# Performance work log

Hardware: AMD Instinct MI355X
Metric: run time of the kernel (lower is better)

## Reference

```python
import jax, jax.numpy as jnp
import numpy as np
from jax import lax

DIM = 128      # per-head dim == channel dim of input
HEADS = 8
INNER = DIM * HEADS
KSZ = 3        # proj_kernel
PAD = KSZ // 2
B = 8
X = 4096       # sequence length
EPS = 1e-5     # BatchNorm eps
SCALE = DIM ** -0.5


def _dw_block(x, dw_w, bn_g, bn_b, bn_m, bn_v, pw_w, pad):
    """DepthWiseConv1d: depthwise conv -> eval-mode BN -> 1x1 conv (no bias).
    x: (n, dim, L); dw_w: (dim, 1, k); pw_w: (out, dim)."""
    dim = dw_w.shape[0]
    y = lax.conv_general_dilated(x, dw_w, (1,), [(pad, pad)],
                                 dimension_numbers=('NCH', 'OIH', 'NCH'),
                                 feature_group_count=dim)
    y = (y - bn_m[:, None]) * (bn_g[:, None] * lax.rsqrt(bn_v[:, None] + EPS)) + bn_b[:, None]
    return jnp.einsum('oi,nix->nox', pw_w, y)


def setup_inputs() -> dict:
    key = jax.random.key(0)
    ks = iter(jax.random.split(key, 40))
    d = {'x': jax.random.normal(next(ks), (B, DIM, X), dtype=jnp.float32)}
    for p in ('q', 'k', 'v'):
        d[p + '_dw'] = jax.random.normal(next(ks), (DIM, 1, KSZ), dtype=jnp.float32) * 0.3
        d[p + '_g'] = 1.0 + 0.1 * jax.random.normal(next(ks), (DIM,), dtype=jnp.float32)
        d[p + '_b'] = 0.1 * jax.random.normal(next(ks), (DIM,), dtype=jnp.float32)
        d[p + '_m'] = 0.1 * jax.random.normal(next(ks), (DIM,), dtype=jnp.float32)
        d[p + '_v'] = jax.random.uniform(next(ks), (DIM,), dtype=jnp.float32, minval=0.5, maxval=1.5)
        d[p + '_pw'] = jax.random.normal(next(ks), (INNER, DIM), dtype=jnp.float32) * (DIM ** -0.5)
    # gating DWConv (dim -> dim, kernel 1, no bias)
    d['gt_dw'] = jax.random.normal(next(ks), (DIM, 1, 1), dtype=jnp.float32) * 0.3
    d['gt_g'] = 1.0 + 0.1 * jax.random.normal(next(ks), (DIM,), dtype=jnp.float32)
    d['gt_b'] = 0.1 * jax.random.normal(next(ks), (DIM,), dtype=jnp.float32)
    d['gt_m'] = 0.1 * jax.random.normal(next(ks), (DIM,), dtype=jnp.float32)
    d['gt_v'] = jax.random.uniform(next(ks), (DIM,), dtype=jnp.float32, minval=0.5, maxval=1.5)
    d['gt_pw'] = jax.random.normal(next(ks), (DIM, DIM), dtype=jnp.float32) * (DIM ** -0.5)
    # to_out 1x1 conv (inner -> dim) with bias
    d['out_w'] = jax.random.normal(next(ks), (DIM, INNER), dtype=jnp.float32) * (INNER ** -0.5)
    d['out_b'] = 0.1 * jax.random.normal(next(ks), (DIM,), dtype=jnp.float32)
    return d


def _split_heads(t):
    # (b, h*d, x) -> (b*h, x, d)
    return t.reshape(B, HEADS, DIM, X).transpose(0, 1, 3, 2).reshape(B * HEADS, X, DIM)


def reference(x, q_dw, q_g, q_b, q_m, q_v, q_pw,
              k_dw, k_g, k_b, k_m, k_v, k_pw,
              v_dw, v_g, v_b, v_m, v_v, v_pw,
              gt_dw, gt_g, gt_b, gt_m, gt_v, gt_pw,
              out_w, out_b):
    q = _split_heads(_dw_block(x, q_dw, q_g, q_b, q_m, q_v, q_pw, PAD))  # (n, x, d)
    k = _split_heads(_dw_block(x, k_dw, k_g, k_b, k_m, k_v, k_pw, PAD))
    v = _split_heads(_dw_block(x, v_dw, v_g, v_b, v_m, v_v, v_pw, PAD))
    # k <- q^T @ softmax(k, axis=-1) * scale : (n, d, d)
    kat = jnp.einsum('nxd,nxe->nde', q, jax.nn.softmax(k, axis=-1)) * SCALE
    # gate: sigmoid(DWConv(q^T)^T) * v
    g_out = _dw_block(q.transpose(0, 2, 1), gt_dw, gt_g, gt_b, gt_m, gt_v, gt_pw, 0)  # (n, d, x)
    gate = jax.nn.sigmoid(g_out.transpose(0, 2, 1)) * v                  # (n, x, d)
    out = jnp.einsum('nxd,nde->nxe', v, kat) + gate                      # (n, x, d)
    out = out.reshape(B, HEADS, X, DIM).transpose(0, 1, 3, 2).reshape(B, INNER, X)
    return jnp.einsum('oi,nix->nox', out_w, out) + out_b[:, None]        # (b, dim, x)
```

## Files before the change

### kernel.cpp

```cpp
#include <hip/hip_runtime.h>
#include <hip/hip_bf16.h>

#define DIMC   128
#define HEADS  8
#define BATCH  8
#define XLEN   4096
#define NHEAD  64
#define EPSV   1e-5f
#define SCALEF 0.08838834764831845f
#define TX     64

typedef __attribute__((ext_vector_type(8))) short bf16x8;
typedef __attribute__((ext_vector_type(4))) float f32x4;
#define MFMA(a,b,c) __builtin_amdgcn_mfma_f32_16x16x32_bf16((a),(b),(c),0,0,0)
#define LDW(tbl, kt, nt) (*(const bf16x8*)&(tbl)[(((kt) * 8 + (nt)) * 64 + l) * 8])

__device__ __forceinline__ short f2bf(float f) {
  union { float f; unsigned u; } v; v.f = f;
  return (short)((v.u + 0x7fffu + ((v.u >> 16) & 1u)) >> 16);
}
__device__ __forceinline__ float bf2f(short h) {
  union { unsigned u; float f; } v; v.u = ((unsigned)(unsigned short)h) << 16;
  return v.f;
}
__device__ __forceinline__ unsigned pk2(float a, float b) {
  return (unsigned)(unsigned short)f2bf(a) | ((unsigned)(unsigned short)f2bf(b) << 16);
}

__device__ __forceinline__ bf16x8 ldY(const short* Y, int row, int kcb) {
  return *(const bf16x8*)((const char*)Y + row*256 + (kcb ^ ((row&7)<<4)));
}

__global__ void k_prep1(const float* dw0, const float* g0, const float* b0, const float* m0, const float* v0,
                        const float* dw1, const float* g1, const float* b1, const float* m1, const float* v1,
                        const float* dw2, const float* g2, const float* b2, const float* m2, const float* v2,
                        const float* gt_pw, const float* gt_dw, const float* gt_g,
                        const float* gt_b, const float* gt_m, const float* gt_v,
                        float* __restrict__ dwf, float* __restrict__ bfl,
                        float* __restrict__ Gt, float* __restrict__ c0) {
  int p = blockIdx.x, c = threadIdx.x;
  if (p < 3) {
    const float* dw = p == 0 ? dw0 : p == 1 ? dw1 : dw2;
    const float* g  = p == 0 ? g0  : p == 1 ? g1  : g2;
    const float* bb = p == 0 ? b0  : p == 1 ? b1  : b2;
    const float* m  = p == 0 ? m0  : p == 1 ? m1  : m2;
    const float* vv = p == 0 ? v0  : p == 1 ? v1  : v2;
    float a = g[c] * rsqrtf(vv[c] + EPSV);
    dwf[(p * DIMC + c) * 3 + 0] = dw[c * 3 + 0] * a;
    dwf[(p * DIMC + c) * 3 + 1] = dw[c * 3 + 1] * a;
    dwf[(p * DIMC + c) * 3 + 2] = dw[c * 3 + 2] * a;
    bfl[p * DIMC + c] = bb[c] - m[c] * a;
  } else {
    int d = c;
    float s = 0.f;
    for (int i = 0; i < DIMC; ++i) {
      float a  = gt_g[i] * rsqrtf(gt_v[i] + EPSV);
      float w1 = gt_dw[i] * a;
      float w0 = gt_b[i] - gt_m[i] * a;
      float pw = gt_pw[d * DIMC + i];
      Gt[i * DIMC + d] = pw * w1;
      s += pw * w0;
    }
    c0[d] = s;
  }
}

__global__ void k_wg(const float* __restrict__ q_pw, const float* __restrict__ Gt,
                     float* __restrict__ WgF) {
  const int h = blockIdx.x, cb = blockIdx.y, t = threadIdx.x;
  const int c = cb * 16 + (t >> 4);
  const int e0 = (t & 15) * 8;
  float acc[8] = {0.f,0.f,0.f,0.f,0.f,0.f,0.f,0.f};
  for (int d = 0; d < DIMC; ++d) {
    float wq = q_pw[((size_t)(h * DIMC + d)) * DIMC + c];
    const float* gr = Gt + d * DIMC + e0;
    #pragma unroll
    for (int j = 0; j < 8; ++j) acc[j] += wq * gr[j];
  }
  float* out = WgF + ((size_t)h * DIMC + c) * DIMC + e0;
  #pragma unroll
  for (int j = 0; j < 8; ++j) out[j] = acc[j];
}

__global__ void k_pack(const float* __restrict__ q_pw, const float* __restrict__ k_pw,
                       const float* __restrict__ v_pw, const float* __restrict__ out_w,
                       const float* __restrict__ WgF,
                       short* __restrict__ Wpk, short* __restrict__ Opk,
                       short* __restrict__ Gpk) {
  const int blk = blockIdx.x, t = threadIdx.x;
  if (blk < 48) {
    const int p = blk / 16, h = (blk / 2) & 7, hl = blk & 1;
    const float* pw = p == 0 ? q_pw : p == 1 ? k_pw : v_pw;
    short* dst = Wpk + (size_t)((p * 8 + h) * 2 + hl) * 16384;
    for (int s = t; s < 2048; s += 256) {
      const int l = s & 63, kt = (s >> 6) >> 3, nt = (s >> 6) & 7;
      const int o = h * DIMC + nt * 16 + (l & 15);
      const int cb = kt * 32 + (l >> 4) * 8;
      #pragma unroll
      for (int j = 0; j < 8; ++j) {
        float wv = pw[(size_t)o * DIMC + cb + j];
        short hi = f2bf(wv);
        dst[s * 8 + j] = (hl == 0) ? hi : f2bf(wv - bf2f(hi));
      }
    }
  } else if (blk < 64) {
    const int m = blk - 48, h = m >> 1, hl = m & 1;
    short* dst = Opk + (size_t)(h * 2 + hl) * 16384;
    for (int s = t; s < 2048; s += 256) {
      const int l = s & 63, mt = (s >> 6) >> 2, kt = (s >> 6) & 3;
      const int o = mt * 16 + (l & 15);
      const int ib = h * DIMC + kt * 32 + (l >> 4) * 8;
      #pragma unroll
      for (int j = 0; j < 8; ++j) {
        float wv = out_w[(size_t)o * (DIMC * HEADS) + ib + j];
        short hi = f2bf(wv);
        dst[s * 8 + j] = (hl == 0) ? hi : f2bf(wv - bf2f(hi));
      }
    }
  } else {
    const int h = blk - 64;
    const float* src = WgF + (size_t)h * 16384;
    short* dst = Gpk + (size_t)h * 16384;
    for (int s = t; s < 2048; s += 256) {
      const int l = s & 63, kt = (s >> 6) >> 3, nt = (s >> 6) & 7;
      const int cb = kt * 32 + (l >> 4) * 8, e = nt * 16 + (l & 15);
      #pragma unroll
      for (int j = 0; j < 8; ++j) dst[s * 8 + j] = f2bf(src[(size_t)(cb + j) * DIMC + e]);
    }
  }
}

__global__ __launch_bounds__(256) void k_red(const short* __restrict__ part16,
                                             short* __restrict__ katpk, int splits) {
  __shared__ float sm[DIMC * DIMC];
  const int n = blockIdx.x, t = threadIdx.x;
  for (int i0 = t * 8; i0 < DIMC * DIMC; i0 += 256 * 8) {
    float a[8] = {0.f,0.f,0.f,0.f,0.f,0.f,0.f,0.f};
    for (int s8 = 0; s8 < splits; ++s8) {
      bf16x8 pv = *(const bf16x8*)&part16[((size_t)(s8 * NHEAD + n)) * 16384 + i0];
      #pragma unroll
      for (int j = 0; j < 8; ++j) a[j] += bf2f(pv[j]);
    }
    #pragma unroll
    for (int j = 0; j < 8; ++j) sm[i0 + j] = a[j] * SCALEF;
  }
  __syncthreads();
  short* dst = katpk + (size_t)n * 16384;
  for (int s = t; s < 2048; s += 256) {
    const int l = s & 63, kt = (s >> 6) >> 3, nt = (s >> 6) & 7;
    const int db = kt * 32 + (l >> 4) * 8, e = nt * 16 + (l & 15);
    #pragma unroll
    for (int j = 0; j < 8; ++j) dst[s * 8 + j] = f2bf(sm[(db + j) * DIMC + e]);
  }
}

__device__ __forceinline__ void stage2(const float* __restrict__ x,
    const float* __restrict__ dwf, const float* __restrict__ bfl,
    int b, int xg0, int t, short* Y0, short* Y1, int p0, int p1)
{
  const int xl = t & 63, cg = t >> 6;
  const int xg = xg0 + xl;
  #pragma unroll
  for (int i = 0; i < 16; ++i) {
    const int c = 2 * (cg + 4 * i);
    float v0[2], v1[2];
    #pragma unroll
    for (int u = 0; u < 2; ++u) {
      const int cc = c + u;
      const float* xr = x + ((size_t)b * DIMC + cc) * XLEN + xg;
      float xm = (xg > 0) ? xr[-1] : 0.f;
      float xc = xr[0];
      float xp = (xg < XLEN - 1) ? xr[1] : 0.f;
      const float* d0 = dwf + (p0 * DIMC + cc) * 3;
      const float* d1 = dwf + (p1 * DIMC + cc) * 3;
      v0[u] = xm * d0[0] + xc * d0[1] + xp * d0[2] + bfl[p0 * DIMC + cc];
      v1[u] = xm * d1[0] + xc * d1[1] + xp * d1[2] + bfl[p1 * DIMC + cc];
    }
    const unsigned off = xl * 256 + ((c * 2) ^ ((xl & 7) << 4));
    *(unsigned*)((char*)Y0 + off) = pk2(v0[0], v0[1]);
    *(unsigned*)((char*)Y1 + off) = pk2(v1[0], v1[1]);
  }
}

__global__ __launch_bounds__(256) void k_proj(
    const float* __restrict__ x, const float* __restrict__ dwf,
    const float* __restrict__ bfl, const short* __restrict__ Wpk,
    short* __restrict__ qT, short* __restrict__ sT, int b)
{
  __shared__ __align__(16) short Yq[TX * 128], Yk[TX * 128];
  __shared__ __align__(16) short QT[128 * TX], ST[128 * TX];
  const int t = threadIdx.x, w = t >> 6, l = t & 63;
  const int l15 = l & 15, lq = l >> 4;
  const int h = blockIdx.y;
  const int x0 = blockIdx.x * TX;

  stage2(x, dwf, bfl, b, x0, t, Yq, Yk, 0, 1);
  __syncthreads();

  const short* WqHi = Wpk + (size_t)((0 * 8 + h) * 2 + 0) * 16384;
  const short* WkHi = Wpk + (size_t)((1 * 8 + h) * 2 + 0) * 16384;

  f32x4 qa[8];

  #pragma unroll
  for (int j = 0; j < 8; ++j) qa[j] = {0.f, 0.f, 0.f, 0.f};
  {
    bf16x8 a0 = ldY(Yq, w * 16 + l15, 0 * 64 + lq * 16);
    bf16x8 a1 = ldY(Yq, w * 16 + l15, 1 * 64 + lq * 16);
    bf16x8 a2 = ldY(Yq, w * 16 + l15, 2 * 64 + lq * 16);
    bf16x8 a3 = ldY(Yq, w * 16 + l15, 3 * 64 + lq * 16);
    bf16x8 h0[8], h1[8];
    #pragma unroll
    for (int nt = 0; nt < 8; ++nt) h0[nt] = LDW(WqHi, 0, nt);
    #pragma unroll
    for (int nt = 0; nt < 8; ++nt) h1[nt] = LDW(WqHi, 1, nt);
    #pragma unroll
    for (int nt = 0; nt < 8; ++nt) qa[nt] = MFMA(a0, h0[nt], qa[nt]);
    #pragma unroll
    for (int nt = 0; nt < 8; ++nt) h0[nt] = LDW(WqHi, 2, nt);
    #pragma unroll
    for (int nt = 0; nt < 8; ++nt) qa[nt] = MFMA(a1, h1[nt], qa[nt]);
    #pragma unroll
    for (int nt = 0; nt < 8; ++nt) h1[nt] = LDW(WqHi, 3, nt);
    #pragma unroll
    for (int nt = 0; nt < 8; ++nt) qa[nt] = MFMA(a2, h0[nt], qa[nt]);
    #pragma unroll
    for (int nt = 0; nt < 8; ++nt) qa[nt] = MFMA(a3, h1[nt], qa[nt]);
  }
  #pragma unroll
  for (int nt = 0; nt < 8; ++nt) {
    const int d = nt * 16 + l15;
    #pragma unroll
    for (int rp = 0; rp < 2; ++rp) {
      const int x2 = w * 16 + lq * 4 + rp * 2;
      *(unsigned*)((char*)QT + d * 128 + ((x2 * 2) ^ ((d & 7) << 4))) =
          pk2(qa[nt][rp * 2], qa[nt][rp * 2 + 1]);
    }
  }

  #pragma unroll
  for (int j = 0; j < 8; ++j) qa[j] = {0.f, 0.f, 0.f, 0.f};
  {
    bf16x8 a0 = ldY(Yk, w * 16 + l15, 0 * 64 + lq * 16);
    bf16x8 a1 = ldY(Yk, w * 16 + l15, 1 * 64 + lq * 16);
    bf16x8 a2 = ldY(Yk, w * 16 + l15, 2 * 64 + lq * 16);
    bf16x8 a3 = ldY(Yk, w * 16 + l15, 3 * 64 + lq * 16);
    bf16x8 h0[8], h1[8];
    #pragma unroll
    for (int nt = 0; nt < 8; ++nt) h0[nt] = LDW(WkHi, 0, nt);
    #pragma unroll
    for (int nt = 0; nt < 8; ++nt) h1[nt] = LDW(WkHi, 1, nt);
    #pragma unroll
    for (int nt = 0; nt < 8; ++nt) qa[nt] = MFMA(a0, h0[nt], qa[nt]);
    #pragma unroll
    for (int nt = 0; nt < 8; ++nt) h0[nt] = LDW(WkHi, 2, nt);
    #pragma unroll
    for (int nt = 0; nt < 8; ++nt) qa[nt] = MFMA(a1, h1[nt], qa[nt]);
    #pragma unroll
    for (int nt = 0; nt < 8; ++nt) h1[nt] = LDW(WkHi, 3, nt);
    #pragma unroll
    for (int nt = 0; nt < 8; ++nt) qa[nt] = MFMA(a2, h0[nt], qa[nt]);
    #pragma unroll
    for (int nt = 0; nt < 8; ++nt) qa[nt] = MFMA(a3, h1[nt], qa[nt]);
  }
  float inv[4];
  #pragma unroll
  for (int r = 0; r < 4; ++r) {
    float m = qa[0][r];
    #pragma unroll
    for (int nt = 1; nt < 8; ++nt) m = fmaxf(m, qa[nt][r]);
    m = fmaxf(m, __shfl_xor(m, 1)); m = fmaxf(m, __shfl_xor(m, 2));
    m = fmaxf(m, __shfl_xor(m, 4)); m = fmaxf(m, __shfl_xor(m, 8));
    float s = 0.f;
    #pragma unroll
    for (int nt = 0; nt < 8; ++nt) { float e = __expf(qa[nt][r] - m); qa[nt][r] = e; s += e; }
    s += __shfl_xor(s, 1); s += __shfl_xor(s, 2); s += __shfl_xor(s, 4); s += __shfl_xor(s, 8);
    inv[r] = 1.f / s;
  }
  #pragma unroll
  for (int nt = 0; nt < 8; ++nt) {
    const int e = nt * 16 + l15;
    #pragma unroll
    for (int rp = 0; rp < 2; ++rp) {
      const int x2 = w * 16 + lq * 4 + rp * 2;
      *(unsigned*)((char*)ST + e * 128 + ((x2 * 2) ^ ((e & 7) << 4))) =
          pk2(qa[nt][rp * 2] * inv[rp * 2], qa[nt][rp * 2 + 1] * inv[rp * 2 + 1]);
    }
  }
  __syncthreads();

  {
    const int r = t >> 1, half = t & 1;
    const size_t row = ((size_t)h * DIMC + r) * XLEN + x0 + half * 32;
    #pragma unroll
    for (int i = 0; i < 4; ++i) {
      const int off = r * 128 + (((half * 64) + i * 16) ^ ((r & 7) << 4));
      *(int4*)(qT + row + i * 8) = *(const int4*)((const char*)QT + off);
      *(int4*)(sT + row + i * 8) = *(const int4*)((const char*)ST + off);
    }
  }
}

__global__ __launch_bounds__(256) void k_katg(
    const short* __restrict__ qT, const short* __restrict__ sT,
    short* __restrict__ part16, int b)
{
  __shared__ __align__(16) short QL[128 * 128];
  __shared__ __align__(16) short SL[32 * 128];
  const int t = threadIdx.x, w = t >> 6, l = t & 63;
  const int l15 = l & 15, lq = l >> 4;
  const int h = blockIdx.y, eq = blockIdx.z;
  const int n = b * HEADS + h;
  const int xspan = XLEN / gridDim.x;

  f32x4 ka[2][2];
  #pragma unroll
  for (int i = 0; i < 2; ++i)
    #pragma unroll
    for (int j = 0; j < 2; ++j) ka[i][j] = {0.f, 0.f, 0.f, 0.f};

  for (int ch = 0; ch < xspan / 128; ++ch) {
    const int xl0 = blockIdx.x * xspan + ch * 128;
    __syncthreads();
    #pragma unroll
    for (int R = 0; R < 8; ++R) {
      const int idx = R * 256 + t;
      const int d = idx >> 4, c = idx & 15;
      const size_t rb = (((size_t)h * DIMC + d) * XLEN + xl0) * 2;
      *(int4*)((char*)QL + idx * 16) =
          *(const int4*)((const char*)qT + rb + ((c * 16) ^ ((d & 7) << 4)));
    }
    #pragma unroll
    for (int R = 0; R < 2; ++R) {
      const int idx = R * 256 + t;
      const int er = idx >> 4, c = idx & 15;
      const size_t rb = (((size_t)h * DIMC + eq * 32 + er) * XLEN + xl0) * 2;
      *(int4*)((char*)SL + idx * 16) =
          *(const int4*)((const char*)sT + rb + ((c * 16) ^ ((er & 7) << 4)));
    }
    __syncthreads();
    #pragma unroll
    for (int kt2 = 0; kt2 < 4; ++kt2) {
      bf16x8 a0 = ldY(QL, w * 32 + l15,      kt2 * 64 + lq * 16);
      bf16x8 a1 = ldY(QL, w * 32 + 16 + l15, kt2 * 64 + lq * 16);
      #pragma unroll
      for (int nt = 0; nt < 2; ++nt) {
        bf16x8 bs = ldY(SL, nt * 16 + l15, kt2 * 64 + lq * 16);
        ka[0][nt] = MFMA(a0, bs, ka[0][nt]);
        ka[1][nt] = MFMA(a1, bs, ka[1][nt]);
      }
    }
  }
  short* dst = part16 + ((size_t)(blockIdx.x * NHEAD + n)) * 16384;
  #pragma unroll
  for (int mt = 0; mt < 2; ++mt)
    #pragma unroll
    for (int nt = 0; nt < 2; ++nt)
      #pragma unroll
      for (int r = 0; r < 4; ++r) {
        const int d = w * 32 + mt * 16 + lq * 4 + r;
        const int e = eq * 32 + nt * 16 + l15;
        dst[d * DIMC + e] = f2bf(ka[mt][nt][r]);
      }
}

__global__ __launch_bounds__(256) void k_out11(
    const float* __restrict__ x, const float* __restrict__ dwf,
    const float* __restrict__ bfl, const short* __restrict__ Wpk,
    const short* __restrict__ Gpk, const short* __restrict__ katpk,
    const short* __restrict__ Opk, const float* __restrict__ c0,
    const float* __restrict__ outb, float* __restrict__ outp)
{
  __shared__ __align__(16) short Yq[TX * 128], Yv[TX * 128];
  __shared__ __align__(16) short Vx[TX * 128], Tn[TX * 128];
  const int t = threadIdx.x, w = t >> 6, l = t & 63;
  const int l15 = l & 15, lq = l >> 4;
  const int b = blockIdx.y;
  const int x0 = blockIdx.x * TX;

  f32x4 oacc[2][4];
  #pragma unroll
  for (int i = 0; i < 2; ++i)
    #pragma unroll
    for (int j = 0; j < 4; ++j) oacc[i][j] = {0.f, 0.f, 0.f, 0.f};
  float c0v[8];
  #pragma unroll
  for (int nt = 0; nt < 8; ++nt) c0v[nt] = c0[nt * 16 + l15];

  stage2(x, dwf, bfl, b, x0, t, Yq, Yv, 0, 2);
  __syncthreads();

  for (int h = 0; h < HEADS; ++h) {
    const int n = b * HEADS + h;
    const short* WvHi = Wpk + (size_t)((2 * 8 + h) * 2 + 0) * 16384;
    const short* Wg   = Gpk + (size_t)h * 16384;
    const short* Kp   = katpk + (size_t)n * 16384;
    const short* OHi  = Opk + (size_t)(h * 2 + 0) * 16384;

    bf16x8 P0[8], P1[8], Q0[8], Q1[8];
    #pragma unroll
    for (int i = 0; i < 8; ++i) P0[i] = LDW(WvHi, 0, i);
    #pragma unroll
    for (int i = 0; i < 8; ++i) P1[i] = LDW(WvHi, 1, i);
    #pragma unroll
    for (int i = 0; i < 8; ++i) Q0[i] = LDW(WvHi, 2, i);
    #pragma unroll
    for (int i = 0; i < 8; ++i) Q1[i] = LDW(WvHi, 3, i);

    f32x4 va[8];
    #pragma unroll
    for (int j = 0; j < 8; ++j) va[j] = {0.f, 0.f, 0.f, 0.f};
    {
      bf16x8 a = ldY(Yv, w * 16 + l15, 0 * 64 + lq * 16);
      #pragma unroll
      for (int nt = 0; nt < 8; ++nt) va[nt] = MFMA(a, P0[nt], va[nt]);
    }
    #pragma unroll
    for (int i = 0; i < 8; ++i) P0[i] = LDW(Wg, 0, i);
    {
      bf16x8 a = ldY(Yv, w * 16 + l15, 1 * 64 + lq * 16);
      #pragma unroll
      for (int nt = 0; nt < 8; ++nt) va[nt] = MFMA(a, P1[nt], va[nt]);
    }
    #pragma unroll
    for (int i = 0; i < 8; ++i) P1[i] = LDW(Wg, 1, i);
    {
      bf16x8 a = ldY(Yv, w * 16 + l15, 2 * 64 + lq * 16);
      #pragma unroll
      for (int nt = 0; nt < 8; ++nt) va[nt] = MFMA(a, Q0[nt], va[nt]);
    }
    #pragma unroll
    for (int i = 0; i < 8; ++i) Q0[i] = LDW(Wg, 2, i);
    {
      bf16x8 a = ldY(Yv, w * 16 + l15, 3 * 64 + lq * 16);
      #pragma unroll
      for (int nt = 0; nt < 8; ++nt) va[nt] = MFMA(a, Q1[nt], va[nt]);
    }
    #pragma unroll
    for (int i = 0; i < 8; ++i) Q1[i] = LDW(Wg, 3, i);

    #pragma unroll
    for (int nt = 0; nt < 8; ++nt) {
      const int dd = nt * 16 + l15;
      #pragma unroll
      for (int r = 0; r < 4; ++r) {
        const int xr = w * 16 + lq * 4 + r;
        *(short*)((char*)Vx + xr * 256 + ((dd * 2) ^ ((xr & 7) << 4))) = f2bf(va[nt][r]);
      }
    }

    f32x4 ga[8];
    #pragma unroll
    for (int j = 0; j < 8; ++j) ga[j] = {0.f, 0.f, 0.f, 0.f};
    {
      bf16x8 a = ldY(Yq, w * 16 + l15, 0 * 64 + lq * 16);
      #pragma unroll
      for (int nt = 0; nt < 8; ++nt) ga[nt] = MFMA(a, P0[nt], ga[nt]);
    }
    #pragma unroll
    for (int i = 0; i < 8; ++i) P0[i] = LDW(Kp, 0, i);
    {
      bf16x8 a = ldY(Yq, w * 16 + l15, 1 * 64 + lq * 16);
      #pragma unroll
      for (int nt = 0; nt < 8; ++nt) ga[nt] = MFMA(a, P1[nt], ga[nt]);
    }
    #pragma unroll
    for (int i = 0; i < 8; ++i) P1[i] = LDW(Kp, 1, i);
    {
      bf16x8 a = ldY(Yq, w * 16 + l15, 2 * 64 + lq * 16);
      #pragma unroll
      for (int nt = 0; nt < 8; ++nt) ga[nt] = MFMA(a, Q0[nt], ga[nt]);
    }
    #pragma unroll
    for (int i = 0; i < 8; ++i) Q0[i] = LDW(Kp, 2, i);
    {
      bf16x8 a = ldY(Yq, w * 16 + l15, 3 * 64 + lq * 16);
      #pragma unroll
      for (int nt = 0; nt < 8; ++nt) ga[nt] = MFMA(a, Q1[nt], ga[nt]);
    }
    #pragma unroll
    for (int i = 0; i < 8; ++i) Q1[i] = LDW(Kp, 3, i);

    #pragma unroll
    for (int nt = 0; nt < 8; ++nt)
      #pragma unroll
      for (int r = 0; r < 4; ++r)
        ga[nt][r] = 1.f / (1.f + __expf(-(ga[nt][r] + c0v[nt])));

    f32x4 kv[8];
    #pragma unroll
    for (int j = 0; j < 8; ++j) kv[j] = {0.f, 0.f, 0.f, 0.f};
    {
      bf16x8 a = ldY(Vx, w * 16 + l15, 0 * 64 + lq * 16);
      #pragma unroll
      for (int nt = 0; nt < 8; ++nt) kv[nt] = MFMA(a, P0[nt], kv[nt]);
    }
    #pragma unroll
    for (int i = 0; i < 8; ++i)
      P0[i] = (*(const bf16x8*)&OHi[((((w * 2 + (i >> 2)) * 4 + (i & 3))) * 64 + l) * 8]);
    {
      bf16x8 a = ldY(Vx, w * 16 + l15, 1 * 64 + lq * 16);
      #pragma unroll
      for (int nt = 0; nt < 8; ++nt) kv[nt] = MFMA(a, P1[nt], kv[nt]);
    }
    {
      bf16x8 a = ldY(Vx, w * 16 + l15, 2 * 64 + lq * 16);
      #pragma unroll
      for (int nt = 0; nt < 8; ++nt) kv[nt] = MFMA(a, Q0[nt], kv[nt]);
    }
    {
      bf16x8 a = ldY(Vx, w * 16 + l15, 3 * 64 + lq * 16);
      #pragma unroll
      for (int nt = 0; nt < 8; ++nt) kv[nt] = MFMA(a, Q1[nt], kv[nt]);
    }

    #pragma unroll
    for (int nt = 0; nt < 8; ++nt) {
      const int e = nt * 16 + l15;
      #pragma unroll
      for (int r = 0; r < 4; ++r) {
        const int xr = w * 16 + lq * 4 + r;
        float vv = bf2f(*(const short*)((const char*)Vx + xr * 256 + ((e * 2) ^ ((xr & 7) << 4))));
        *(short*)((char*)Tn + xr * 256 + ((e * 2) ^ ((xr & 7) << 4))) =
            f2bf(kv[nt][r] + ga[nt][r] * vv);
      }
    }
    __syncthreads();

    #pragma unroll
    for (int kt = 0; kt < 4; ++kt) {
      #pragma unroll
      for (int nt4 = 0; nt4 < 4; ++nt4) {
        bf16x8 bt = ldY(Tn, nt4 * 16 + l15, kt * 64 + lq * 16);
        oacc[0][nt4] = MFMA(P0[0 * 4 + kt], bt, oacc[0][nt4]);
        oacc[1][nt4] = MFMA(P0[1 * 4 + kt], bt, oacc[1][nt4]);
      }
    }
    __syncthreads();
  }
  #pragma unroll
  for (int mt = 0; mt < 2; ++mt) {
    #pragma unroll
    for (int nt4 = 0; nt4 < 4; ++nt4) {
      #pragma unroll
      for (int r = 0; r < 4; ++r) {
        const int o = w * 32 + mt * 16 + lq * 4 + r;
        const int xx = x0 + nt4 * 16 + l15;
        outp[((size_t)b * DIMC + o) * XLEN + xx] = oacc[mt][nt4][r] + outb[o];
      }
    }
  }
}

extern "C" void kernel_launch(void* const* d_in, const int* in_sizes, int n_in,
                              void* d_out, int out_size, void* d_ws, size_t ws_size,
                              hipStream_t stream) {
  (void)in_sizes; (void)n_in; (void)out_size;
  const float* x = (const float*)d_in[0];

  char* ws = (char*)d_ws;
  short* katpk = (short*)(ws);
  short* Wpk   = (short*)(ws + 2097152);
  short* Opk   = (short*)(ws + 3670016);
  short* Gpk   = (short*)(ws + 4194304);
  float* WgF   = (float*)(ws + 4456448);
  float* Gt    = (float*)(ws + 4980736);
  float* c0    = (float*)(ws + 5046272);
  float* dwf   = (float*)(ws + 5046784);
  float* bfl   = (float*)(ws + 5051392);
  constexpr size_t BASE = 5052928;
  const int splits = (ws_size >= (size_t)38607360) ? 8 : 4;
  short* part16 = (short*)(ws + BASE);
  short* qT = (short*)(ws + BASE + (size_t)splits * 2097152);
  short* sT = (short*)((char*)qT + 8388608);
  if (ws_size < (size_t)30218752) return;

  k_prep1<<<4, 128, 0, stream>>>(
      (const float*)d_in[1],  (const float*)d_in[2],  (const float*)d_in[3],
      (const float*)d_in[4],  (const float*)d_in[5],
      (const float*)d_in[7],  (const float*)d_in[8],  (const float*)d_in[9],
      (const float*)d_in[10], (const float*)d_in[11],
      (const float*)d_in[13], (const float*)d_in[14], (const float*)d_in[15],
      (const float*)d_in[16], (const float*)d_in[17],
      (const float*)d_in[24], (const float*)d_in[19], (const float*)d_in[20],
      (const float*)d_in[21], (const float*)d_in[22], (const float*)d_in[23],
      dwf, bfl, Gt, c0);

  k_wg<<<dim3(8, 8), 256, 0, stream>>>((const float*)d_in[6], Gt, WgF);

  k_pack<<<72, 256, 0, stream>>>((const float*)d_in[6], (const float*)d_in[12],
                                 (const float*)d_in[18], (const float*)d_in[25],
                                 WgF, Wpk, Opk, Gpk);

  for (int b = 0; b < BATCH; ++b) {
    k_proj<<<dim3(XLEN / TX, HEADS), 256, 0, stream>>>(x, dwf, bfl, Wpk, qT, sT, b);
    k_katg<<<dim3(splits, HEADS, 4), 256, 0, stream>>>(qT, sT, part16, b);
  }
  k_red<<<NHEAD, 256, 0, stream>>>(part16, katpk, splits);
  k_out11<<<dim3(XLEN / TX, BATCH), 256, 0, stream>>>(x, dwf, bfl, Wpk, Gpk, katpk,
                                                      Opk, c0, (const float*)d_in[26],
                                                      (float*)d_out);
}
```

Measured before the change: 409.5 us.

## Stop packing bf16 low halves; split kat tiles into narrower e-quarters

The weight packing kernel no longer writes the bf16 residual (lo) halves for the projection and output weights, so it launches fewer blocks. Any consumer that still reads the lo slots now sees stale or uninitialised data unless it was already ignoring them. The kat kernel now covers 16 e-columns per block instead of 32 and launches twice as many blocks in z. This raises parallelism but reloads the full Q tile into shared memory twice as often.

```diff
diff --git a/kernel.cpp b/kernel.cpp
--- a/kernel.cpp
+++ b/kernel.cpp
@@ -88,37 +88,31 @@
                        short* __restrict__ Wpk, short* __restrict__ Opk,
                        short* __restrict__ Gpk) {
   const int blk = blockIdx.x, t = threadIdx.x;
-  if (blk < 48) {
-    const int p = blk / 16, h = (blk / 2) & 7, hl = blk & 1;
+  if (blk < 24) {
+    const int p = blk / 8, h = blk & 7;
     const float* pw = p == 0 ? q_pw : p == 1 ? k_pw : v_pw;
-    short* dst = Wpk + (size_t)((p * 8 + h) * 2 + hl) * 16384;
+    short* dst = Wpk + (size_t)((p * 8 + h) * 2 + 0) * 16384;
     for (int s = t; s < 2048; s += 256) {
       const int l = s & 63, kt = (s >> 6) >> 3, nt = (s >> 6) & 7;
       const int o = h * DIMC + nt * 16 + (l & 15);
       const int cb = kt * 32 + (l >> 4) * 8;
       #pragma unroll
-      for (int j = 0; j < 8; ++j) {
-        float wv = pw[(size_t)o * DIMC + cb + j];
-        short hi = f2bf(wv);
-        dst[s * 8 + j] = (hl == 0) ? hi : f2bf(wv - bf2f(hi));
-      }
-    }
-  } else if (blk < 64) {
-    const int m = blk - 48, h = m >> 1, hl = m & 1;
-    short* dst = Opk + (size_t)(h * 2 + hl) * 16384;
+      for (int j = 0; j < 8; ++j)
+        dst[s * 8 + j] = f2bf(pw[(size_t)o * DIMC + cb + j]);
+    }
+  } else if (blk < 32) {
+    const int h = blk - 24;
+    short* dst = Opk + (size_t)(h * 2 + 0) * 16384;
     for (int s = t; s < 2048; s += 256) {
       const int l = s & 63, mt = (s >> 6) >> 2, kt = (s >> 6) & 3;
       const int o = mt * 16 + (l & 15);
       const int ib = h * DIMC + kt * 32 + (l >> 4) * 8;
       #pragma unroll
-      for (int j = 0; j < 8; ++j) {
-        float wv = out_w[(size_t)o * (DIMC * HEADS) + ib + j];
-        short hi = f2bf(wv);
-        dst[s * 8 + j] = (hl == 0) ? hi : f2bf(wv - bf2f(hi));
-      }
+      for (int j = 0; j < 8; ++j)
+        dst[s * 8 + j] = f2bf(out_w[(size_t)o * (DIMC * HEADS) + ib + j]);
     }
   } else {
-    const int h = blk - 64;
+    const int h = blk - 32;
     const float* src = WgF + (size_t)h * 16384;
     short* dst = Gpk + (size_t)h * 16384;
     for (int s = t; s < 2048; s += 256) {
@@ -306,18 +300,16 @@
     short* __restrict__ part16, int b)
 {
   __shared__ __align__(16) short QL[128 * 128];
-  __shared__ __align__(16) short SL[32 * 128];
+  __shared__ __align__(16) short SL[16 * 128];
   const int t = threadIdx.x, w = t >> 6, l = t & 63;
   const int l15 = l & 15, lq = l >> 4;
   const int h = blockIdx.y, eq = blockIdx.z;
   const int n = b * HEADS + h;
   const int xspan = XLEN / gridDim.x;
 
-  f32x4 ka[2][2];
-  #pragma unroll
-  for (int i = 0; i < 2; ++i)
-    #pragma unroll
-    for (int j = 0; j < 2; ++j) ka[i][j] = {0.f, 0.f, 0.f, 0.f};
+  f32x4 ka[2];
+  ka[0] = {0.f, 0.f, 0.f, 0.f};
+  ka[1] = {0.f, 0.f, 0.f, 0.f};
 
   for (int ch = 0; ch < xspan / 128; ++ch) {
     const int xl0 = blockIdx.x * xspan + ch * 128;
@@ -330,11 +322,10 @@
       *(int4*)((char*)QL + idx * 16) =
           *(const int4*)((const char*)qT + rb + ((c * 16) ^ ((d & 7) << 4)));
     }
-    #pragma unroll
-    for (int R = 0; R < 2; ++R) {
-      const int idx = R * 256 + t;
+    {
+      const int idx = t;
       const int er = idx >> 4, c = idx & 15;
-      const size_t rb = (((size_t)h * DIMC + eq * 32 + er) * XLEN + xl0) * 2;
+      const size_t rb = (((size_t)h * DIMC + eq * 16 + er) * XLEN + xl0) * 2;
       *(int4*)((char*)SL + idx * 16) =
           *(const int4*)((const char*)sT + rb + ((c * 16) ^ ((er & 7) << 4)));
     }
@@ -343,25 +334,20 @@
     for (int kt2 = 0; kt2 < 4; ++kt2) {
       bf16x8 a0 = ldY(QL, w * 32 + l15,      kt2 * 64 + lq * 16);
       bf16x8 a1 = ldY(QL, w * 32 + 16 + l15, kt2 * 64 + lq * 16);
-      #pragma unroll
-      for (int nt = 0; nt < 2; ++nt) {
-        bf16x8 bs = ldY(SL, nt * 16 + l15, kt2 * 64 + lq * 16);
-        ka[0][nt] = MFMA(a0, bs, ka[0][nt]);
-        ka[1][nt] = MFMA(a1, bs, ka[1][nt]);
-      }
+      bf16x8 bs = ldY(SL, l15, kt2 * 64 + lq * 16);
+      ka[0] = MFMA(a0, bs, ka[0]);
+      ka[1] = MFMA(a1, bs, ka[1]);
     }
   }
   short* dst = part16 + ((size_t)(blockIdx.x * NHEAD + n)) * 16384;
   #pragma unroll
   for (int mt = 0; mt < 2; ++mt)
     #pragma unroll
-    for (int nt = 0; nt < 2; ++nt)
-      #pragma unroll
-      for (int r = 0; r < 4; ++r) {
-        const int d = w * 32 + mt * 16 + lq * 4 + r;
-        const int e = eq * 32 + nt * 16 + l15;
-        dst[d * DIMC + e] = f2bf(ka[mt][nt][r]);
-      }
+    for (int r = 0; r < 4; ++r) {
+      const int d = w * 32 + mt * 16 + lq * 4 + r;
+      const int e = eq * 16 + l15;
+      dst[d * DIMC + e] = f2bf(ka[mt][r]);
+    }
 }
 
 __global__ __launch_bounds__(256) void k_out11(
@@ -588,13 +574,13 @@
 
   k_wg<<<dim3(8, 8), 256, 0, stream>>>((const float*)d_in[6], Gt, WgF);
 
-  k_pack<<<72, 256, 0, stream>>>((const float*)d_in[6], (const float*)d_in[12],
+  k_pack<<<40, 256, 0, stream>>>((const float*)d_in[6], (const float*)d_in[12],
                                  (const float*)d_in[18], (const float*)d_in[25],
                                  WgF, Wpk, Opk, Gpk);
 
   for (int b = 0; b < BATCH; ++b) {
     k_proj<<<dim3(XLEN / TX, HEADS), 256, 0, stream>>>(x, dwf, bfl, Wpk, qT, sT, b);
-    k_katg<<<dim3(splits, HEADS, 4), 256, 0, stream>>>(qT, sT, part16, b);
+    k_katg<<<dim3(splits, HEADS, 8), 256, 0, stream>>>(qT, sT, part16, b);
   }
   k_red<<<NHEAD, 256, 0, stream>>>(part16, katpk, splits);
   k_out11<<<dim3(XLEN / TX, BATCH), 256, 0, stream>>>(x, dwf, bfl, Wpk, Gpk, katpk,
```

Result: faster. 399.5 us (-2.4%).
